# Performance work log

Hardware: AMD Instinct MI355X
Metric: run time of the kernel (lower is better)

## Reference

```python
import jax, jax.numpy as jnp
import numpy as np

BS, SL, CL = 32, 512, 20      # batch, seq_len (visits), codes per visit
D, H, V = 256, 4, 20000       # d_model, heads, vocab_size
HD = D // H                   # size_per_head = 64
EPS = 1e-5


def make_pe_table(d_model, max_pos):
    # torch PositionalEncoding: sinusoidal table with a zero pad row prepended
    pe = np.array([[pos / np.power(10000, 2.0 * (j // 2) / d_model)
                    for j in range(d_model)] for pos in range(max_pos)])
    pe[:, 0::2] = np.sin(pe[:, 0::2])
    pe[:, 1::2] = np.cos(pe[:, 1::2])
    pe = np.concatenate([np.zeros((1, d_model)), pe], axis=0)
    return jnp.asarray(pe, dtype=jnp.float32)  # [max_pos+1, d]


def layer_norm(x, g, b):
    mu = jnp.mean(x, axis=-1, keepdims=True)
    var = jnp.mean(jnp.square(x - mu), axis=-1, keepdims=True)
    return (x - mu) * jax.lax.rsqrt(var + EPS) * g + b


def setup_inputs() -> dict:
    key = jax.random.key(0)
    ks = jax.random.split(key, 12)
    input_seqs = jax.random.randint(ks[0], (BS, SL, CL), 0, V, dtype=jnp.int32)
    masks = jnp.ones((BS, SL, SL), dtype=jnp.int32)
    lengths = jax.random.randint(ks[1], (BS,), 1, SL + 1, dtype=jnp.int32)
    seq_time_step = jax.random.uniform(ks[2], (BS, SL), dtype=jnp.float32)
    code_masks = jax.random.uniform(ks[3], (BS, SL, CL), dtype=jnp.float32)

    emb_table = jax.random.normal(ks[4], (V + 1, D), dtype=jnp.float32) * 0.02
    emb_table = emb_table.at[V].set(0.0)  # padding_idx row (never indexed here)
    bound = 1.0 / np.sqrt(V)
    bias_emb = jax.random.uniform(ks[5], (D,), minval=-bound, maxval=bound, dtype=jnp.float32)
    s = 1.0 / np.sqrt(D)
    Wq = jax.random.uniform(ks[6], (D, D), minval=-s, maxval=s, dtype=jnp.float32)
    Wk = jax.random.uniform(ks[7], (D, D), minval=-s, maxval=s, dtype=jnp.float32)
    Wv = jax.random.uniform(ks[8], (D, D), minval=-s, maxval=s, dtype=jnp.float32)
    Wfc = jax.random.uniform(ks[9], (D, D), minval=-s, maxval=s, dtype=jnp.float32)
    ln_g = jnp.ones((D,), dtype=jnp.float32)
    ln_b = jnp.zeros((D,), dtype=jnp.float32)
    so = 1.0 / np.sqrt(4 * D)
    out_w = jax.random.uniform(ks[10], (2, 4 * D), minval=-so, maxval=so, dtype=jnp.float32)
    out_b = jax.random.uniform(ks[11], (2,), minval=-so, maxval=so, dtype=jnp.float32)
    pe_table = make_pe_table(D, SL)

    return dict(input_seqs=input_seqs, masks=masks, lengths=lengths,
                seq_time_step=seq_time_step, code_masks=code_masks,
                emb_table=emb_table, bias_emb=bias_emb, pe_table=pe_table,
                Wq=Wq, Wk=Wk, Wv=Wv, Wfc=Wfc, ln_g=ln_g, ln_b=ln_b,
                out_w=out_w, out_b=out_b)


def reference(input_seqs, masks, lengths, seq_time_step, code_masks,
              emb_table, bias_emb, pe_table, Wq, Wk, Wv, Wfc,
              ln_g, ln_b, out_w, out_b):
    bs, sl, _ = input_seqs.shape
    # visit embedding: sum of code embeddings + bias  -> [bs, sl, d]
    x = emb_table[input_seqs].sum(axis=2) + bias_emb
    # positional encoding: pos ids = 1..len, 0 beyond length
    t_idx = jnp.arange(sl, dtype=jnp.int32)
    pos_ids = jnp.where(t_idx[None, :] < lengths[:, None], t_idx[None, :] + 1, 0)
    x = x + pe_table[pos_ids]
    res = x
    # manual MHA -- NOTE faithful to original: view(bs, H, sl, hd) directly
    q = (x @ Wq.T).reshape(bs, H, sl, HD)
    k = (x @ Wk.T).reshape(bs, H, sl, HD)
    v = (x @ Wv.T).reshape(bs, H, sl, HD)
    energy = jnp.einsum('bhqd,bhkd->bhqk', q, k) / np.sqrt(HD)
    energy = jnp.where(masks[:, None, :, :] == 0, -jnp.inf, energy)
    attn = jax.nn.softmax(energy, axis=-1)
    o = jnp.einsum('bhqk,bhkd->bhqd', attn, v)          # [bs,H,sl,hd]
    o = o.transpose(0, 2, 1, 3).reshape(bs, sl, D)
    x = layer_norm(o @ Wfc.T + res, ln_g, ln_b)
    # zero out positions >= length
    valid = (t_idx[None, :] < lengths[:, None])          # [bs, sl]
    x = jnp.where(valid[:, :, None], x, 0.0)
    # triangular-weighted temporal pooling into 4 bins (vectorized loops)
    lens = lengths.astype(jnp.float32)
    t = jnp.arange(1, sl + 1, dtype=jnp.float32)
    s_val = 4.0 * t[None, :] / lens[:, None]             # [bs, sl]
    m = jnp.arange(1, 5, dtype=jnp.float32)              # 4 bins
    w = jnp.square(1.0 - jnp.abs(s_val[:, :, None] - m[None, None, :]) / 4.0)  # [bs,sl,4]
    U = jnp.einsum('bsm,bsd->bmd', w, x)                 # [bs,4,d]
    U = U.reshape(bs, 4 * D)
    return U @ out_w.T + out_b                           # [bs, 2]
```

## Files before the change

### kernel.cpp

```cpp
#include <hip/hip_runtime.h>

#define BSZ 32
#define SLEN 512
#define CLEN 20
#define DMOD 256
#define NH 4
#define HDIM 64

typedef _Float16 half8 __attribute__((ext_vector_type(8)));
typedef _Float16 half4 __attribute__((ext_vector_type(4)));
typedef float float4v __attribute__((ext_vector_type(4)));

#define MFMA16(a, b, c) __builtin_amdgcn_mfma_f32_16x16x32_f16(a, b, c, 0, 0, 0)
#define PG(fi) ((((fi) >> 4) * 17) + ((fi) & 15))

__global__ __launch_bounds__(256) void k_cast(
    const float* __restrict__ W0, const float* __restrict__ W1,
    const float* __restrict__ W2, const float* __restrict__ W3,
    const float* __restrict__ emb,
    _Float16* __restrict__ wh, _Float16* __restrict__ embh) {
  const int bid = blockIdx.x;
  const float* src;
  _Float16* dst;
  int idx;
  if (bid < 128) {
    const int z = bid >> 5;
    src = (z == 0) ? W0 : (z == 1) ? W1 : (z == 2) ? W2 : W3;
    dst = wh + (size_t)z * 65536;
    idx = ((bid & 31) * 256 + threadIdx.x) * 8;
  } else {
    src = emb;
    dst = embh;
    idx = ((bid - 128) * 256 + threadIdx.x) * 8;
  }
  float v[8];
  *(float4*)v = *(const float4*)(src + idx);
  *(float4*)(v + 4) = *(const float4*)(src + idx + 4);
  half8 h;
  #pragma unroll
  for (int i = 0; i < 8; ++i) h[i] = (_Float16)v[i];
  *(half8*)(dst + idx) = h;
}

__global__ __launch_bounds__(256) void k_embmask(
    const int* __restrict__ seqs, const int* __restrict__ lengths,
    const _Float16* __restrict__ embh, const float* __restrict__ bias,
    const float* __restrict__ pe, _Float16* __restrict__ x,
    const int* __restrict__ masks, unsigned int* __restrict__ pk) {
  const int row0 = blockIdx.x * 8;
  const int sub = threadIdx.x >> 5;
  const int hl = threadIdx.x & 31;
  const int row = row0 + sub;
  const int b = row >> 9, s = row & 511;
  __shared__ int codes[8][CLEN];
  if (threadIdx.x < 8 * CLEN)
    codes[threadIdx.x / CLEN][threadIdx.x % CLEN] = seqs[row0 * CLEN + threadIdx.x];
  __syncthreads();
  const int pos = (s < lengths[b]) ? (s + 1) : 0;
  const int d = hl * 8;
  float acc[8];
  *(float4*)acc = *(const float4*)(bias + d);
  *(float4*)(acc + 4) = *(const float4*)(bias + d + 4);
  const float4 pv0 = *(const float4*)(pe + (size_t)pos * DMOD + d);
  const float4 pv1 = *(const float4*)(pe + (size_t)pos * DMOD + d + 4);
  acc[0] += pv0.x; acc[1] += pv0.y; acc[2] += pv0.z; acc[3] += pv0.w;
  acc[4] += pv1.x; acc[5] += pv1.y; acc[6] += pv1.z; acc[7] += pv1.w;
  #pragma unroll
  for (int c = 0; c < CLEN; ++c) {
    const half8 ev = *(const half8*)(embh + (size_t)codes[sub][c] * DMOD + d);
    #pragma unroll
    for (int i = 0; i < 8; ++i) acc[i] += (float)ev[i];
  }
  half8 hv;
  #pragma unroll
  for (int i = 0; i < 8; ++i) hv[i] = (_Float16)acc[i];
  *(half8*)(x + (size_t)row * DMOD + d) = hv;
  const int wv = threadIdx.x >> 6;
  const int lane = threadIdx.x & 63;
  #pragma unroll
  for (int p = 0; p < 16; ++p) {
    const int it = wv + p * 4;
    const int r = row0 + (it >> 3);
    const int chunk = it & 7;
    const int m = masks[(size_t)r * SLEN + chunk * 64 + lane];
    const unsigned long long bal = __ballot(m != 0);
    if (lane == 0) {
      pk[(size_t)r * 16 + chunk * 2]     = (unsigned int)bal;
      pk[(size_t)r * 16 + chunk * 2 + 1] = (unsigned int)(bal >> 32);
    }
  }
}

__global__ __launch_bounds__(256) void k_gemm_qkv(
    const _Float16* __restrict__ A, const _Float16* __restrict__ Wb,
    _Float16* __restrict__ q, _Float16* __restrict__ k, _Float16* __restrict__ v) {
  const int z = blockIdx.z;
  _Float16* Cb = (z == 0) ? q : (z == 1) ? k : v;
  const _Float16* w_ = Wb + (size_t)z * 65536;
  const int m0 = blockIdx.x * 128;
  const int n0 = blockIdx.y * 128;
  const int tid = threadIdx.x;
  const int lane = tid & 63;
  const int w = tid >> 6;
  const int wm = (w >> 1) * 4;
  const int wn = (w & 1) * 4;
  __shared__ _Float16 smem[8704];
  half8* As = (half8*)(smem);
  half8* Ws = (half8*)(smem + 4096);
  float4v acc[4][4];
  #pragma unroll
  for (int i = 0; i < 4; ++i)
    #pragma unroll
    for (int j = 0; j < 4; ++j)
      acc[i][j] = (float4v){0.f, 0.f, 0.f, 0.f};
  int li_[2]; size_t ga_[2], gw_[2];
  #pragma unroll
  for (int p = 0; p < 2; ++p) {
    const int c = tid + p * 256;
    const int r = c & 127, qd = c >> 7;
    li_[p] = (r >> 4) * 64 + qd * 16 + (r & 15);
    ga_[p] = (size_t)(m0 + r) * DMOD + qd * 8;
    gw_[p] = (size_t)(n0 + r) * DMOD + qd * 8;
  }
  half8 pa[2], pw[2];
  #pragma unroll
  for (int p = 0; p < 2; ++p) {
    pa[p] = *(const half8*)(A + ga_[p]);
    pw[p] = *(const half8*)(w_ + gw_[p]);
  }
  for (int k0 = 0; k0 < DMOD; k0 += 32) {
    #pragma unroll
    for (int p = 0; p < 2; ++p) {
      As[li_[p]] = pa[p];
      Ws[li_[p]] = pw[p];
    }
    __syncthreads();
    if (k0 + 32 < DMOD) {
      #pragma unroll
      for (int p = 0; p < 2; ++p) {
        pa[p] = *(const half8*)(A + ga_[p] + k0 + 32);
        pw[p] = *(const half8*)(w_ + gw_[p] + k0 + 32);
      }
    }
    half8 af[4], wf[4];
    #pragma unroll
    for (int i = 0; i < 4; ++i) {
      af[i] = As[(wm + i) * 64 + lane];
      wf[i] = Ws[(wn + i) * 64 + lane];
    }
    #pragma unroll
    for (int i = 0; i < 4; ++i)
      #pragma unroll
      for (int j = 0; j < 4; ++j)
        acc[i][j] = MFMA16(af[i], wf[j], acc[i][j]);
    __syncthreads();
  }
  const int cr = (lane >> 4) * 4;
  const int cc = lane & 15;
  _Float16* Eh = smem;
  #pragma unroll
  for (int ip = 0; ip < 4; ++ip) {
    #pragma unroll
    for (int j = 0; j < 4; ++j) {
      const int col = (wn + j) * 16 + cc;
      #pragma unroll
      for (int r = 0; r < 4; ++r)
        Eh[((w >> 1) * 16 + cr + r) * 136 + col] = (_Float16)acc[ip][j][r];
    }
    __syncthreads();
    #pragma unroll
    for (int e = 0; e < 2; ++e) {
      const int idx = tid + e * 256;
      const int lr = idx >> 4;
      const int cg = idx & 15;
      const int gr = m0 + (lr >> 4) * 64 + ip * 16 + (lr & 15);
      *(half8*)(Cb + (size_t)gr * DMOD + n0 + cg * 8) =
          *(const half8*)&Eh[lr * 136 + cg * 8];
    }
    __syncthreads();
  }
}

__global__ __launch_bounds__(256) void k_vt(
    const _Float16* __restrict__ v, _Float16* __restrict__ vt) {
  const int bh = blockIdx.x;
  const size_t off = (size_t)bh * 32768;
  __shared__ _Float16 Th[64][66];
  const int tid = threadIdx.x;
  const int sc = blockIdx.y * 64;
  #pragma unroll
  for (int p = 0; p < 2; ++p) {
    const int lin = tid + p * 256;
    const int r = lin >> 3, g = lin & 7;
    *(half8*)&Th[r][g * 8] = *(const half8*)(v + off + (size_t)(sc + r) * 64 + g * 8);
  }
  __syncthreads();
  #pragma unroll
  for (int p = 0; p < 2; ++p) {
    const int lin = tid + p * 256;
    const int d = lin >> 3, sg = lin & 7;
    half8 hv;
    #pragma unroll
    for (int j = 0; j < 8; ++j) hv[j] = Th[sg * 8 + j][d];
    *(half8*)(vt + off + (size_t)d * 512 + sc + sg * 8) = hv;
  }
}

__global__ __launch_bounds__(256) void k_fcln(
    const _Float16* __restrict__ A, const _Float16* __restrict__ w_,
    const _Float16* __restrict__ res, const int* __restrict__ lengths,
    const float* __restrict__ g, const float* __restrict__ bb,
    float* __restrict__ Up) {
  const int m0 = blockIdx.x * 64;
  const int b = m0 >> 9;
  const int s0 = m0 & 511;
  const int tid = threadIdx.x;
  const int lane = tid & 63;
  const int w = tid >> 6;
  __shared__ half8 As[256], Ws[1024];
  __shared__ float Rs[4][64], Rq[4][64];
  __shared__ float Fmu[64], Fiv[64];
  float4v acc[4][4];
  #pragma unroll
  for (int i = 0; i < 4; ++i)
    #pragma unroll
    for (int j = 0; j < 4; ++j)
      acc[i][j] = (float4v){0.f, 0.f, 0.f, 0.f};
  const int ra = tid & 63, qa = tid >> 6;
  const int li_a = (ra >> 4) * 64 + qa * 16 + (ra & 15);
  const size_t ga_ = (size_t)(m0 + ra) * DMOD + qa * 8;
  int li_w[4]; size_t gw_[4];
  #pragma unroll
  for (int p = 0; p < 4; ++p) {
    const int c = tid + p * 256;
    const int rw = c & 255, qw = c >> 8;
    li_w[p] = (rw >> 4) * 64 + qw * 16 + (rw & 15);
    gw_[p] = (size_t)rw * DMOD + qw * 8;
  }
  half8 pa = *(const half8*)(A + ga_);
  half8 pw[4];
  #pragma unroll
  for (int p = 0; p < 4; ++p) pw[p] = *(const half8*)(w_ + gw_[p]);
  for (int k0 = 0; k0 < DMOD; k0 += 32) {
    As[li_a] = pa;
    #pragma unroll
    for (int p = 0; p < 4; ++p) Ws[li_w[p]] = pw[p];
    __syncthreads();
    if (k0 + 32 < DMOD) {
      pa = *(const half8*)(A + ga_ + k0 + 32);
      #pragma unroll
      for (int p = 0; p < 4; ++p) pw[p] = *(const half8*)(w_ + gw_[p] + k0 + 32);
    }
    half8 af[4], wf[4];
    #pragma unroll
    for (int i = 0; i < 4; ++i) {
      af[i] = As[i * 64 + lane];
      wf[i] = Ws[(w * 4 + i) * 64 + lane];
    }
    #pragma unroll
    for (int i = 0; i < 4; ++i)
      #pragma unroll
      for (int j = 0; j < 4; ++j)
        acc[i][j] = MFMA16(af[i], wf[j], acc[i][j]);
    __syncthreads();
  }
  const int cr = (lane >> 4) * 4;
  const int cc = lane & 15;
  const int l15 = cc;
  #pragma unroll
  for (int i = 0; i < 4; ++i)
    #pragma unroll
    for (int j = 0; j < 4; ++j) {
      const int col = (w * 4 + j) * 16 + cc;
      #pragma unroll
      for (int r = 0; r < 4; ++r)
        acc[i][j][r] += (float)res[(size_t)(m0 + i * 16 + cr + r) * DMOD + col];
    }
  float S[4][4], Q2[4][4];
  #pragma unroll
  for (int i = 0; i < 4; ++i)
    #pragma unroll
    for (int r = 0; r < 4; ++r) {
      float s = 0.f, q2 = 0.f;
      #pragma unroll
      for (int j = 0; j < 4; ++j) {
        const float v = acc[i][j][r];
        s += v; q2 += v * v;
      }
      #pragma unroll
      for (int off = 1; off <= 8; off <<= 1) {
        s += __shfl_xor(s, off);
        q2 += __shfl_xor(q2, off);
      }
      S[i][r] = s; Q2[i][r] = q2;
    }
  if (l15 == 0) {
    #pragma unroll
    for (int i = 0; i < 4; ++i)
      #pragma unroll
      for (int r = 0; r < 4; ++r) {
        Rs[w][i * 16 + cr + r] = S[i][r];
        Rq[w][i * 16 + cr + r] = Q2[i][r];
      }
  }
  __syncthreads();
  if (tid < 64) {
    const float s = Rs[0][tid] + Rs[1][tid] + Rs[2][tid] + Rs[3][tid];
    const float q2 = Rq[0][tid] + Rq[1][tid] + Rq[2][tid] + Rq[3][tid];
    const float mu = s * (1.0f / DMOD);
    Fmu[tid] = mu;
    Fiv[tid] = rsqrtf(q2 * (1.0f / DMOD) - mu * mu + 1e-5f);
  }
  __syncthreads();
  const int len = lengths[b];
  const float inv4 = 4.0f / (float)len;
  float gl[4], bl[4];
  #pragma unroll
  for (int j = 0; j < 4; ++j) {
    const int col = (w * 4 + j) * 16 + cc;
    gl[j] = g[col]; bl[j] = bb[col];
  }
  float pool[4][4] = {};
  #pragma unroll
  for (int i = 0; i < 4; ++i)
    #pragma unroll
    for (int r = 0; r < 4; ++r) {
      const int row_l = i * 16 + cr + r;
      const int sg = s0 + row_l;
      const bool valid = sg < len;
      const float mu = Fmu[row_l], iv = Fiv[row_l];
      const float sv = (float)(sg + 1) * inv4;
      float t2[4];
      #pragma unroll
      for (int m = 0; m < 4; ++m) {
        const float tm = 1.0f - fabsf(sv - (float)(m + 1)) * 0.25f;
        t2[m] = tm * tm;
      }
      #pragma unroll
      for (int j = 0; j < 4; ++j) {
        const float ov = valid ? (acc[i][j][r] - mu) * iv * gl[j] + bl[j] : 0.f;
        #pragma unroll
        for (int m = 0; m < 4; ++m) pool[m][j] += t2[m] * ov;
      }
    }
  #pragma unroll
  for (int m = 0; m < 4; ++m)
    #pragma unroll
    for (int j = 0; j < 4; ++j) {
      pool[m][j] += __shfl_xor(pool[m][j], 16);
      pool[m][j] += __shfl_xor(pool[m][j], 32);
    }
  const int sc = (m0 >> 6) & 7;
  if ((lane >> 4) == 0) {
    #pragma unroll
    for (int m = 0; m < 4; ++m)
      #pragma unroll
      for (int j = 0; j < 4; ++j)
        Up[(((size_t)b * 8 + sc) * 4 + m) * DMOD + (w * 4 + j) * 16 + cc] =
            pool[m][j];
  }
}

__global__ __launch_bounds__(256, 2) void k_attn(
    const _Float16* __restrict__ q_, const _Float16* __restrict__ k_,
    const _Float16* __restrict__ vt, const unsigned int* __restrict__ pk,
    _Float16* __restrict__ o) {
  const int L = blockIdx.x;
  const int bh = (L & 7) * 16 + ((L >> 3) & 15);
  const int q0 = (L >> 7) * 128;
  const size_t bhoff = (size_t)bh * 32768;
  __shared__ half8 QP[1088];
  __shared__ half8 Ks[544], Vs[544];
  __shared__ unsigned long long Ms64[128];
  __shared__ float Ps[4][128];
  __shared__ float lsum[128];
  const int tid = threadIdx.x;
  const int w = tid >> 6;
  const int lane = tid & 63;
  const int l15 = lane & 15;
  const int quad = lane >> 4;
  #pragma unroll
  for (int p = 0; p < 4; ++p) {
    const int lin = tid + p * 256;
    const int r = lin >> 3, g = lin & 7;
    const int fi = (r >> 4) * 128 + g * 16 + (r & 15);
    QP[PG(fi)] = *(const half8*)(q_ + bhoff + (size_t)(q0 + r) * 64 + g * 8);
  }
  __syncthreads();
  half8 qf[8][2];
  #pragma unroll
  for (int ns = 0; ns < 8; ++ns) {
    const int gq = ns * 8 + quad;
    qf[ns][0] = QP[gq * 17 + l15];
    qf[ns][1] = QP[(gq + 4) * 17 + l15];
  }
  float4v oacc[8];
  float lsw[8] = {0.f, 0.f, 0.f, 0.f, 0.f, 0.f, 0.f, 0.f};
  #pragma unroll
  for (int ns = 0; ns < 8; ++ns) oacc[ns] = (float4v){0.f, 0.f, 0.f, 0.f};
  for (int kc = 0; kc < SLEN; kc += 64) {
    __syncthreads();
    #pragma unroll
    for (int p = 0; p < 2; ++p) {
      const int lin = tid + p * 256;
      const int r = lin >> 3, g = lin & 7;
      const int fi = PG((r >> 4) * 128 + g * 16 + (r & 15));
      Ks[fi] = *(const half8*)(k_ + bhoff + (size_t)(kc + r) * 64 + g * 8);
      Vs[fi] = *(const half8*)(vt + bhoff + (size_t)r * 512 + kc + g * 8);
    }
    ((unsigned int*)Ms64)[tid] =
        pk[((size_t)((bh >> 2) << 9) + q0 + (tid >> 1)) * 16 + (kc >> 5) + (tid & 1)];
    __syncthreads();
    const int ga0 = (w * 8 + quad) * 17 + l15;
    const int ga1 = (w * 8 + quad + 4) * 17 + l15;
    const half8 ah0 = Ks[ga0], ah1 = Ks[ga1];
    #pragma unroll
    for (int ns = 0; ns < 8; ++ns) {
      float4v s = (float4v){0.f, 0.f, 0.f, 0.f};
      s = MFMA16(ah0, qf[ns][0], s);
      s = MFMA16(ah1, qf[ns][1], s);
      const int q = ns * 16 + l15;
      const unsigned long long mrow = Ms64[q];
      const unsigned mbits = (unsigned)(mrow >> (w * 16 + quad * 4)) & 15u;
      half4 h4;
      #pragma unroll
      for (int r = 0; r < 4; ++r) {
        const float pe = ((mbits >> r) & 1u) ? __expf(s[r] * 0.125f) : 0.f;
        h4[r] = (_Float16)pe;
        lsw[ns] += pe;
      }
      const int hb = ((ns * 8 + w * 2 + (quad >> 1)) * 17 + l15) * 8 + (quad & 1) * 4;
      *(half4*)((_Float16*)QP + hb) = h4;
    }
    __syncthreads();
    const half8 vh0 = Vs[ga0], vh1 = Vs[ga1];
    #pragma unroll
    for (int ns = 0; ns < 8; ++ns) {
      const int pb0 = (ns * 8 + quad) * 17 + l15;
      const int pb1 = (ns * 8 + quad + 4) * 17 + l15;
      oacc[ns] = MFMA16(vh0, QP[pb0], oacc[ns]);
      oacc[ns] = MFMA16(vh1, QP[pb1], oacc[ns]);
    }
  }
  #pragma unroll
  for (int ns = 0; ns < 8; ++ns) {
    lsw[ns] += __shfl_xor(lsw[ns], 16);
    lsw[ns] += __shfl_xor(lsw[ns], 32);
  }
  __syncthreads();
  if (quad == 0) {
    #pragma unroll
    for (int ns = 0; ns < 8; ++ns) Ps[w][ns * 16 + l15] = lsw[ns];
  }
  __syncthreads();
  if (tid < 128) lsum[tid] = Ps[0][tid] + Ps[1][tid] + Ps[2][tid] + Ps[3][tid];
  __syncthreads();
  const int b = bh >> 2, h = bh & 3;
  _Float16* Ot = (_Float16*)QP;
  #pragma unroll
  for (int ns = 0; ns < 8; ++ns) {
    const int q = ns * 16 + l15;
    const float inv = 1.0f / lsum[q];
    half4 h4;
    #pragma unroll
    for (int r = 0; r < 4; ++r) h4[r] = (_Float16)(oacc[ns][r] * inv);
    *(half4*)&Ot[q * 68 + w * 16 + quad * 4] = h4;
  }
  __syncthreads();
  #pragma unroll
  for (int e = 0; e < 4; ++e) {
    const int idx = tid + e * 256;
    const int qq = idx >> 3, g = idx & 7;
    *(half8*)(o + ((size_t)(b * SLEN + q0 + qq)) * DMOD + h * HDIM + g * 8) =
        *(const half8*)&Ot[qq * 68 + g * 8];
  }
}

__global__ __launch_bounds__(256) void k_out(
    const float* __restrict__ Up, const float* __restrict__ ow,
    const float* __restrict__ ob, float* __restrict__ out) {
  const int b = blockIdx.x;
  const int tid = threadIdx.x;
  const int w = tid >> 6;
  const int lane = tid & 63;
  __shared__ float rr[8];
  float4 s = {0.f, 0.f, 0.f, 0.f};
  #pragma unroll
  for (int c = 0; c < 8; ++c) {
    const float4 u = *(const float4*)(Up + ((size_t)b * 8 + c) * 1024 + tid * 4);
    s.x += u.x; s.y += u.y; s.z += u.z; s.w += u.w;
  }
  const float4 w0 = *(const float4*)(ow + tid * 4);
  const float4 w1 = *(const float4*)(ow + 1024 + tid * 4);
  float acc0 = s.x * w0.x + s.y * w0.y + s.z * w0.z + s.w * w0.w;
  float acc1 = s.x * w1.x + s.y * w1.y + s.z * w1.z + s.w * w1.w;
  #pragma unroll
  for (int off = 32; off > 0; off >>= 1) {
    acc0 += __shfl_xor(acc0, off);
    acc1 += __shfl_xor(acc1, off);
  }
  if (lane == 0) { rr[w] = acc0; rr[4 + w] = acc1; }
  __syncthreads();
  if (tid == 0) {
    out[b * 2 + 0] = rr[0] + rr[1] + rr[2] + rr[3] + ob[0];
    out[b * 2 + 1] = rr[4] + rr[5] + rr[6] + rr[7] + ob[1];
  }
}

extern "C" void kernel_launch(void* const* d_in, const int* in_sizes, int n_in,
                              void* d_out, int out_size, void* d_ws, size_t ws_size,
                              hipStream_t stream) {
  const int* seqs     = (const int*)d_in[0];
  const int* masks    = (const int*)d_in[1];
  const int* lengths  = (const int*)d_in[2];
  const float* emb    = (const float*)d_in[5];
  const float* bias   = (const float*)d_in[6];
  const float* pe     = (const float*)d_in[7];
  const float* Wq     = (const float*)d_in[8];
  const float* Wk     = (const float*)d_in[9];
  const float* Wv     = (const float*)d_in[10];
  const float* Wfc    = (const float*)d_in[11];
  const float* ln_g   = (const float*)d_in[12];
  const float* ln_b   = (const float*)d_in[13];
  const float* out_w  = (const float*)d_in[14];
  const float* out_b  = (const float*)d_in[15];
  float* outp = (float*)d_out;

  const size_t NE = (size_t)BSZ * SLEN * DMOD;
  _Float16* q = (_Float16*)d_ws;
  _Float16* k = q + NE;
  _Float16* v = k + NE;
  _Float16* vt = v + NE;
  _Float16* x = vt + NE;
  _Float16* o = x + NE;
  _Float16* wh = o + NE;
  unsigned int* pk = (unsigned int*)(wh + 4 * 65536);
  float* Up = (float*)(pk + BSZ * SLEN * 16);
  _Float16* embh = (_Float16*)d_ws;

  k_cast<<<2628, 256, 0, stream>>>(Wq, Wk, Wv, Wfc, emb, wh, embh);
  k_embmask<<<BSZ * SLEN / 8, 256, 0, stream>>>(seqs, lengths, embh, bias, pe, x,
                                                masks, pk);
  k_gemm_qkv<<<dim3(128, 2, 3), 256, 0, stream>>>(x, wh, q, k, v);
  k_vt<<<dim3(BSZ * NH, 8), 256, 0, stream>>>(v, vt);
  k_attn<<<BSZ * NH * (SLEN / 128), 256, 0, stream>>>(q, k, vt, pk, o);
  k_fcln<<<256, 256, 0, stream>>>(o, wh + 3 * 65536, x, lengths, ln_g, ln_b, Up);
  k_out<<<BSZ, 256, 0, stream>>>(Up, out_w, out_b, outp);
}
```

Measured before the change: 217.5 us.

## Double-buffer K/V/mask tiles in attention kernel with register prefetch

The attention kernel's K, V and mask tiles now live in two shared-memory buffers. The next 64-key chunk is loaded into registers while the current chunk's QK MFMAs and exp run, then written to the alternate buffer before the barrier. This aims to hide global-load latency behind compute. In exchange it doubles K/V shared memory and adds register pressure, which could reduce occupancy under launch_bounds(256,2).

```diff
diff --git a/kernel.cpp b/kernel.cpp
--- a/kernel.cpp
+++ b/kernel.cpp
@@ -370,8 +370,8 @@
   const int q0 = (L >> 7) * 128;
   const size_t bhoff = (size_t)bh * 32768;
   __shared__ half8 QP[1088];
-  __shared__ half8 Ks[544], Vs[544];
-  __shared__ unsigned long long Ms64[128];
+  __shared__ half8 Ks[2][544], Vs[2][544];
+  __shared__ unsigned long long Ms64[2][128];
   __shared__ float Ps[4][128];
   __shared__ float lsum[128];
   const int tid = threadIdx.x;
@@ -386,6 +386,16 @@
     const int fi = (r >> 4) * 128 + g * 16 + (r & 15);
     QP[PG(fi)] = *(const half8*)(q_ + bhoff + (size_t)(q0 + r) * 64 + g * 8);
   }
+  int fi_[2]; const _Float16 *ka_[2], *va_[2];
+  #pragma unroll
+  for (int p = 0; p < 2; ++p) {
+    const int lin = tid + p * 256;
+    const int r = lin >> 3, g = lin & 7;
+    fi_[p] = PG((r >> 4) * 128 + g * 16 + (r & 15));
+    ka_[p] = k_ + bhoff + (size_t)r * 64 + g * 8;
+    va_[p] = vt + bhoff + (size_t)r * 512 + g * 8;
+  }
+  const size_t mb_ = ((size_t)((bh >> 2) << 9) + q0 + (tid >> 1)) * 16 + (tid & 1);
   __syncthreads();
   half8 qf[8][2];
   #pragma unroll
@@ -394,33 +404,38 @@
     qf[ns][0] = QP[gq * 17 + l15];
     qf[ns][1] = QP[(gq + 4) * 17 + l15];
   }
+  #pragma unroll
+  for (int p = 0; p < 2; ++p) {
+    Ks[0][fi_[p]] = *(const half8*)(ka_[p]);
+    Vs[0][fi_[p]] = *(const half8*)(va_[p]);
+  }
+  ((unsigned int*)Ms64[0])[tid] = pk[mb_];
+  __syncthreads();
   float4v oacc[8];
   float lsw[8] = {0.f, 0.f, 0.f, 0.f, 0.f, 0.f, 0.f, 0.f};
   #pragma unroll
   for (int ns = 0; ns < 8; ++ns) oacc[ns] = (float4v){0.f, 0.f, 0.f, 0.f};
-  for (int kc = 0; kc < SLEN; kc += 64) {
-    __syncthreads();
-    #pragma unroll
-    for (int p = 0; p < 2; ++p) {
-      const int lin = tid + p * 256;
-      const int r = lin >> 3, g = lin & 7;
-      const int fi = PG((r >> 4) * 128 + g * 16 + (r & 15));
-      Ks[fi] = *(const half8*)(k_ + bhoff + (size_t)(kc + r) * 64 + g * 8);
-      Vs[fi] = *(const half8*)(vt + bhoff + (size_t)r * 512 + kc + g * 8);
-    }
-    ((unsigned int*)Ms64)[tid] =
-        pk[((size_t)((bh >> 2) << 9) + q0 + (tid >> 1)) * 16 + (kc >> 5) + (tid & 1)];
-    __syncthreads();
-    const int ga0 = (w * 8 + quad) * 17 + l15;
-    const int ga1 = (w * 8 + quad + 4) * 17 + l15;
-    const half8 ah0 = Ks[ga0], ah1 = Ks[ga1];
+  const int ga0 = (w * 8 + quad) * 17 + l15;
+  const int ga1 = (w * 8 + quad + 4) * 17 + l15;
+  for (int t = 0; t < 8; ++t) {
+    const int b = t & 1;
+    half8 kr0, kr1, vr0, vr1; unsigned int mreg = 0;
+    if (t < 7) {
+      const int kcn = (t + 1) * 64;
+      kr0 = *(const half8*)(ka_[0] + (size_t)kcn * 64);
+      kr1 = *(const half8*)(ka_[1] + (size_t)kcn * 64);
+      vr0 = *(const half8*)(va_[0] + kcn);
+      vr1 = *(const half8*)(va_[1] + kcn);
+      mreg = pk[mb_ + (kcn >> 5)];
+    }
+    const half8 ah0 = Ks[b][ga0], ah1 = Ks[b][ga1];
     #pragma unroll
     for (int ns = 0; ns < 8; ++ns) {
       float4v s = (float4v){0.f, 0.f, 0.f, 0.f};
       s = MFMA16(ah0, qf[ns][0], s);
       s = MFMA16(ah1, qf[ns][1], s);
       const int q = ns * 16 + l15;
-      const unsigned long long mrow = Ms64[q];
+      const unsigned long long mrow = Ms64[b][q];
       const unsigned mbits = (unsigned)(mrow >> (w * 16 + quad * 4)) & 15u;
       half4 h4;
       #pragma unroll
@@ -432,8 +447,15 @@
       const int hb = ((ns * 8 + w * 2 + (quad >> 1)) * 17 + l15) * 8 + (quad & 1) * 4;
       *(half4*)((_Float16*)QP + hb) = h4;
     }
-    __syncthreads();
-    const half8 vh0 = Vs[ga0], vh1 = Vs[ga1];
+    if (t < 7) {
+      Ks[b ^ 1][fi_[0]] = kr0;
+      Ks[b ^ 1][fi_[1]] = kr1;
+      Vs[b ^ 1][fi_[0]] = vr0;
+      Vs[b ^ 1][fi_[1]] = vr1;
+      ((unsigned int*)Ms64[b ^ 1])[tid] = mreg;
+    }
+    __syncthreads();
+    const half8 vh0 = Vs[b][ga0], vh1 = Vs[b][ga1];
     #pragma unroll
     for (int ns = 0; ns < 8; ++ns) {
       const int pb0 = (ns * 8 + quad) * 17 + l15;
@@ -441,13 +463,13 @@
       oacc[ns] = MFMA16(vh0, QP[pb0], oacc[ns]);
       oacc[ns] = MFMA16(vh1, QP[pb1], oacc[ns]);
     }
+    __syncthreads();
   }
   #pragma unroll
   for (int ns = 0; ns < 8; ++ns) {
     lsw[ns] += __shfl_xor(lsw[ns], 16);
     lsw[ns] += __shfl_xor(lsw[ns], 32);
   }
-  __syncthreads();
   if (quad == 0) {
     #pragma unroll
     for (int ns = 0; ns < 8; ++ns) Ps[w][ns * 16 + l15] = lsw[ns];
```

Result: faster. 210.4 us (-3.3%).
